# Kernel optimization log

Hardware: AMD Instinct MI355X
Metric: run time of the kernel (lower is better)

The kernel has to match this reference:

```python
import jax, jax.numpy as jnp
import numpy as np

HEADS = 12

def setup_inputs() -> dict:
    key = jax.random.key(0)
    k1, k2, k3 = jax.random.split(key, 3)
    b, n, d = 8, 1024, 768
    x = jax.random.normal(k1, (b, n, d), dtype=jnp.float32)
    # xavier_uniform-like init for linear weights
    lim_qkv = float(np.sqrt(6.0 / (d + 3 * d)))
    W_qkv = jax.random.uniform(k2, (3 * d, d), dtype=jnp.float32, minval=-lim_qkv, maxval=lim_qkv)
    b_qkv = jnp.zeros((3 * d,), dtype=jnp.float32)
    lim_o = float(np.sqrt(6.0 / (d + d)))
    W_out = jax.random.uniform(k3, (d, d), dtype=jnp.float32, minval=-lim_o, maxval=lim_o)
    b_out = jnp.zeros((d,), dtype=jnp.float32)
    return {"x": x, "W_qkv": W_qkv, "b_qkv": b_qkv, "W_out": W_out, "b_out": b_out}

def reference(x, W_qkv, b_qkv, W_out, b_out):
    b, n, d = x.shape
    h = HEADS
    hd = d // h
    scale = d ** (-0.5)  # NOTE: original scales by dim**-0.5, not head_dim**-0.5
    qkv = x @ W_qkv.T + b_qkv                      # [b, n, 3d]
    q, k, v = jnp.split(qkv, 3, axis=-1)           # each [b, n, d]
    def to_heads(t):
        return t.reshape(b, n, h, hd).transpose(0, 2, 1, 3)  # [b, h, n, hd]
    q, k, v = to_heads(q), to_heads(k), to_heads(v)
    dots = jnp.einsum('bhid,bhjd->bhij', q, k) * scale       # [b, h, n, n]
    attn = jax.nn.softmax(dots, axis=-1)
    out = jnp.einsum('bhij,bhjd->bhid', attn, v)             # [b, h, n, hd]
    out = out.transpose(0, 2, 1, 3).reshape(b, n, d)
    return out @ W_out.T + b_out
```

## Files before the change

kernel.cpp:

```cpp
#include <hip/hip_runtime.h>
#include <stdint.h>

typedef __bf16 bf16x8 __attribute__((ext_vector_type(8)));
typedef float  f32x4  __attribute__((ext_vector_type(4)));
typedef unsigned short u16;

#define AS1 __attribute__((address_space(1)))
#define AS3 __attribute__((address_space(3)))
#define G2L(gp, lp) __builtin_amdgcn_global_load_lds( \
    (const AS1 unsigned int*)(uintptr_t)(gp), \
    (AS3 unsigned int*)(uintptr_t)(lp), 16, 0, 0)

static __device__ __forceinline__ u16 f32_to_bf16(float f) {
    unsigned u = __float_as_uint(f);
    u += 0x7fffu + ((u >> 16) & 1u);
    return (u16)(u >> 16);
}

static __device__ __forceinline__ unsigned pack_bf16(float lo, float hi) {
    return (unsigned)f32_to_bf16(lo) | ((unsigned)f32_to_bf16(hi) << 16);
}

static __device__ __forceinline__ float fast_exp2(float x) {
    return __builtin_amdgcn_exp2f(x);
}

static __device__ __forceinline__ f32x4 mfma16(bf16x8 a, bf16x8 b, f32x4 c) {
    return __builtin_amdgcn_mfma_f32_16x16x32_bf16(a, b, c, 0, 0, 0);
}

__global__ void cvt3_k(const float* __restrict__ a, const float* __restrict__ b,
                       const float* __restrict__ c, u16* __restrict__ out) {
    const int i = blockIdx.x * blockDim.x + threadIdx.x;
    const float* src; int off;
    if (i < 1572864)      { src = a; off = 0; }
    else if (i < 2015232) { src = b; off = 1572864; }
    else                  { src = c; off = 2015232; }
    const float4 v = reinterpret_cast<const float4*>(src)[i - off];
    reinterpret_cast<uint2*>(out)[i] = make_uint2(pack_bf16(v.x, v.y), pack_bf16(v.z, v.w));
}

template<int OUTF32>
__global__ __launch_bounds__(256, 2) void gemm_bt_k(const u16* __restrict__ A, const u16* __restrict__ B,
                                                    const float* __restrict__ bias, void* __restrict__ Cp,
                                                    int M, int N, int K, int nbx) {
    __shared__ __align__(16) u16 As[2][128 * 64];
    __shared__ __align__(16) u16 Bs[2][128 * 64];
    const int id = blockIdx.x;
    const int cpx = gridDim.x >> 3;
    const int swz = (id & 7) * cpx + (id >> 3);
    const int bx = swz % nbx, by = swz / nbx;
    const int t = threadIdx.x, w = t >> 6, l = t & 63, lr = l & 15, lg = l >> 4;
    const int wr = w >> 1, wc = w & 1;
    const long rowBase = (long)by * 128;
    const long colBase = (long)bx * 128;

    const f32x4 z = {0.f, 0.f, 0.f, 0.f};
    f32x4 acc[4][4];
    #pragma unroll
    for (int m = 0; m < 4; ++m)
        #pragma unroll
        for (int n = 0; n < 4; ++n) acc[m][n] = z;

    const int kSteps = K >> 6;
    #pragma unroll
    for (int i = 0; i < 4; ++i) {
        const int c = i * 256 + t, row = c >> 3, ch = c & 7;
        const int sch = ch ^ (row & 7);
        G2L(A + (rowBase + row) * K + sch * 8, &As[0][(i * 256 + w * 64) * 8]);
        G2L(B + (colBase + row) * K + sch * 8, &Bs[0][(i * 256 + w * 64) * 8]);
    }
    for (int kt = 0; kt < kSteps; ++kt) {
        const int cur = kt & 1;
        asm volatile("s_waitcnt vmcnt(0)" ::: "memory");
        __builtin_amdgcn_sched_barrier(0);
        __builtin_amdgcn_s_barrier();
        __builtin_amdgcn_sched_barrier(0);
        if (kt + 1 < kSteps) {
            const int k0 = (kt + 1) << 6;
            #pragma unroll
            for (int i = 0; i < 4; ++i) {
                const int c = i * 256 + t, row = c >> 3, ch = c & 7;
                const int sch = ch ^ (row & 7);
                G2L(A + (rowBase + row) * K + k0 + sch * 8, &As[cur ^ 1][(i * 256 + w * 64) * 8]);
                G2L(B + (colBase + row) * K + k0 + sch * 8, &Bs[cur ^ 1][(i * 256 + w * 64) * 8]);
            }
        }
        __builtin_amdgcn_sched_barrier(0);
        #pragma unroll
        for (int kk = 0; kk < 2; ++kk) {
            bf16x8 af[4], bfr[4];
            #pragma unroll
            for (int m = 0; m < 4; ++m) {
                const int row = wr * 64 + m * 16 + lr;
                af[m] = *reinterpret_cast<const bf16x8*>(&As[cur][row * 64 + (((kk * 4 + lg) ^ (lr & 7)) << 3)]);
            }
            #pragma unroll
            for (int n = 0; n < 4; ++n) {
                const int row = wc * 64 + n * 16 + lr;
                bfr[n] = *reinterpret_cast<const bf16x8*>(&Bs[cur][row * 64 + (((kk * 4 + lg) ^ (lr & 7)) << 3)]);
            }
            #pragma unroll
            for (int m = 0; m < 4; ++m)
                #pragma unroll
                for (int n = 0; n < 4; ++n) acc[m][n] = mfma16(af[m], bfr[n], acc[m][n]);
        }
    }
    #pragma unroll
    for (int n = 0; n < 4; ++n) {
        const long gc = colBase + wc * 64 + n * 16 + lr;
        const float bv = bias[gc];
        #pragma unroll
        for (int m = 0; m < 4; ++m) {
            const long gr = rowBase + wr * 64 + m * 16 + lg * 4;
            #pragma unroll
            for (int r = 0; r < 4; ++r) {
                const float v = acc[m][n][r] + bv;
                if (OUTF32) reinterpret_cast<float*>(Cp)[(gr + r) * N + gc] = v;
                else        reinterpret_cast<u16*>(Cp)[(gr + r) * N + gc] = f32_to_bf16(v);
            }
        }
    }
}

__global__ __launch_bounds__(256) void transpose_v_k(const u16* __restrict__ qkv, u16* __restrict__ vt) {
    const int bh = blockIdx.y, b = bh / 12, h = bh % 12;
    const int nt = blockIdx.x;
    __shared__ __align__(16) u16 Ts[64][72];
    const int t = threadIdx.x;
    const int rr = t >> 2;
    #pragma unroll
    for (int i = 0; i < 2; ++i) {
        const int ch = (t & 3) + i * 4;
        const u16* src = qkv + (long)(b * 1024 + nt * 64 + rr) * 2304 + 1536 + h * 64 + ch * 8;
        *reinterpret_cast<uint4*>(&Ts[rr][ch * 8]) = *reinterpret_cast<const uint4*>(src);
    }
    __syncthreads();
    #pragma unroll
    for (int i = 0; i < 2; ++i) {
        const int ch = (t & 3) + i * 4;
        u16 vals[8];
        #pragma unroll
        for (int j = 0; j < 8; ++j)
            vals[j] = Ts[(j & 3) * 16 + ch * 2 + (j >> 2)][rr];
        u16* dst = vt + (long)(bh * 64 + rr) * 1024 + nt * 64 + ch * 8;
        *reinterpret_cast<uint4*>(dst) = *reinterpret_cast<const uint4*>(vals);
    }
}

__global__ __launch_bounds__(256, 3) void attn_k(const u16* __restrict__ qkv, const u16* __restrict__ vt,
                                                 u16* __restrict__ outp) {
    const int id = blockIdx.x;
    const int bh = id % 96, qt = id / 96;
    const int b = bh / 12, h = bh % 12;
    const int t = threadIdx.x, w = t >> 6, l = t & 63, lr = l & 15, lg = l >> 4;
    __shared__ __align__(16) u16 Ks[2][64 * 64];
    __shared__ __align__(16) u16 Vts[2][64 * 64];
    __shared__ __align__(16) u16 Ps[8192];

    const u16* kb = qkv + 768 + h * 64;
    const u16* vb = vt + (long)bh * 64 * 1024;

    #pragma unroll
    for (int i = 0; i < 2; ++i) {
        const int c = (i * 4 + w) * 64 + l;
        const int row = c >> 3, sch = (c & 7) ^ (row & 7);
        G2L(kb + (long)(b * 1024 + row) * 2304 + sch * 8, &Ks[0][(i * 4 + w) * 512]);
        G2L(vb + (long)row * 1024 + sch * 8, &Vts[0][(i * 4 + w) * 512]);
    }
    #pragma unroll
    for (int j = 0; j < 4; ++j) {
        const int c = j * 256 + t, row = c >> 3, ch = c & 7;
        const uint4 q = *reinterpret_cast<const uint4*>(
            qkv + (long)(b * 1024 + qt * 128 + row) * 2304 + h * 64 + ch * 8);
        *reinterpret_cast<uint4*>(&Ps[row * 64 + ((ch ^ (row & 7)) << 3)]) = q;
    }
    __syncthreads();
    bf16x8 aq[2][2];
    #pragma unroll
    for (int qg = 0; qg < 2; ++qg)
        #pragma unroll
        for (int kk = 0; kk < 2; ++kk)
            aq[qg][kk] = *reinterpret_cast<const bf16x8*>(
                &Ps[(qg * 64 + w * 16 + lr) * 64 + (((kk * 4 + lg) ^ (lr & 7)) << 3)]);

    const f32x4 z = {0.f, 0.f, 0.f, 0.f};
    f32x4 o[2][4];
    #pragma unroll
    for (int qg = 0; qg < 2; ++qg)
        #pragma unroll
        for (int n = 0; n < 4; ++n) o[qg][n] = z;
    float lacc[2][4] = {{0.f, 0.f, 0.f, 0.f}, {0.f, 0.f, 0.f, 0.f}};
    const float sc2 = 0.052058773f;

    for (int kt = 0; kt < 16; ++kt) {
        const int cur = kt & 1;
        asm volatile("s_waitcnt vmcnt(0)" ::: "memory");
        __builtin_amdgcn_sched_barrier(0);
        __builtin_amdgcn_s_barrier();
        __builtin_amdgcn_sched_barrier(0);
        if (kt < 15) {
            const int ktn = kt + 1;
            #pragma unroll
            for (int i = 0; i < 2; ++i) {
                const int c = (i * 4 + w) * 64 + l;
                const int row = c >> 3, sch = (c & 7) ^ (row & 7);
                G2L(kb + (long)(b * 1024 + ktn * 64 + row) * 2304 + sch * 8, &Ks[cur ^ 1][(i * 4 + w) * 512]);
                G2L(vb + (long)row * 1024 + ktn * 64 + sch * 8, &Vts[cur ^ 1][(i * 4 + w) * 512]);
            }
        }
        __builtin_amdgcn_sched_barrier(0);
        f32x4 s[2][4];
        #pragma unroll
        for (int qg = 0; qg < 2; ++qg)
            #pragma unroll
            for (int kc = 0; kc < 4; ++kc) s[qg][kc] = z;
        #pragma unroll
        for (int kk = 0; kk < 2; ++kk) {
            #pragma unroll
            for (int kc = 0; kc < 4; ++kc) {
                const int row = kc * 16 + lr;
                bf16x8 bk = *reinterpret_cast<const bf16x8*>(&Ks[cur][row * 64 + (((kk * 4 + lg) ^ (lr & 7)) << 3)]);
                s[0][kc] = mfma16(aq[0][kk], bk, s[0][kc]);
                s[1][kc] = mfma16(aq[1][kk], bk, s[1][kc]);
            }
        }
        #pragma unroll
        for (int qg = 0; qg < 2; ++qg) {
            #pragma unroll
            for (int r = 0; r < 4; ++r) {
                const float p0 = fast_exp2(s[qg][0][r] * sc2);
                const float p1 = fast_exp2(s[qg][1][r] * sc2);
                const float p2 = fast_exp2(s[qg][2][r] * sc2);
                const float p3 = fast_exp2(s[qg][3][r] * sc2);
                lacc[qg][r] += (p0 + p1) + (p2 + p3);
                const unsigned w0 = pack_bf16(p0, p1);
                const unsigned w1 = pack_bf16(p2, p3);
                const int q = lg * 4 + r;
                const int csw = (lr >> 1) ^ (q & 7);
                *reinterpret_cast<uint2*>(&Ps[w * 2048 + qg * 1024 + q * 64 + csw * 8 + (lr & 1) * 4]) =
                    make_uint2(w0, w1);
            }
        }
        #pragma unroll
        for (int kk = 0; kk < 2; ++kk) {
            const int swzk = ((kk * 4 + lg) ^ (lr & 7)) << 3;
            bf16x8 pa0 = *reinterpret_cast<const bf16x8*>(&Ps[w * 2048 + lr * 64 + swzk]);
            bf16x8 pa1 = *reinterpret_cast<const bf16x8*>(&Ps[w * 2048 + 1024 + lr * 64 + swzk]);
            #pragma unroll
            for (int n = 0; n < 4; ++n) {
                const int row = n * 16 + lr;
                bf16x8 vbf = *reinterpret_cast<const bf16x8*>(&Vts[cur][row * 64 + swzk]);
                o[0][n] = mfma16(pa0, vbf, o[0][n]);
                o[1][n] = mfma16(pa1, vbf, o[1][n]);
            }
        }
    }
    #pragma unroll
    for (int qg = 0; qg < 2; ++qg) {
        #pragma unroll
        for (int r = 0; r < 4; ++r) {
            float rs = lacc[qg][r];
            #pragma unroll
            for (int off = 1; off < 16; off <<= 1) rs += __shfl_xor(rs, off, 64);
            lacc[qg][r] = rs;
        }
        const int qrow = qt * 128 + qg * 64 + w * 16 + lg * 4;
        #pragma unroll
        for (int n = 0; n < 4; ++n) {
            #pragma unroll
            for (int r = 0; r < 4; ++r) {
                const float v = o[qg][n][r] / lacc[qg][r];
                outp[(long)(b * 1024 + qrow + r) * 768 + h * 64 + n * 16 + lr] = f32_to_bf16(v);
            }
        }
    }
}

extern "C" void kernel_launch(void* const* d_in, const int* in_sizes, int n_in,
                              void* d_out, int out_size, void* d_ws, size_t ws_size,
                              hipStream_t stream) {
    (void)in_sizes; (void)n_in; (void)out_size; (void)ws_size;
    const float* x    = (const float*)d_in[0];
    const float* Wqkv = (const float*)d_in[1];
    const float* bqkv = (const float*)d_in[2];
    const float* Wout = (const float*)d_in[3];
    const float* bout = (const float*)d_in[4];

    u16* xb   = (u16*)d_ws;
    u16* Wqb  = xb  + 6291456;
    u16* Wob  = Wqb + 1769472;
    u16* qkv  = Wob + 589824;
    u16* vtb  = qkv + 18874368;
    u16* attn = vtb + 6291456;

    cvt3_k<<<8448, 256, 0, stream>>>(x, Wqkv, Wout, xb);

    gemm_bt_k<0><<<1152, 256, 0, stream>>>(xb, Wqb, bqkv, qkv, 8192, 2304, 768, 18);
    transpose_v_k<<<dim3(16, 96), 256, 0, stream>>>(qkv, vtb);
    attn_k<<<768, 256, 0, stream>>>(qkv, vtb, attn);
    gemm_bt_k<1><<<384, 256, 0, stream>>>(attn, Wob, bout, d_out, 8192, 768, 768, 6);
}
```

Measured before the change: 114.4 us.

## Keep softmax probabilities in registers via transposed QK MFMA and fold scale into QKV GEMM

The attention kernel now computes S^T (K as the A operand), so each lane's exp'd scores already form the A-operand layout for the PV MFMA. This removes the per-tile LDS round trip through Ps and the Q staging in LDS. Row sums are computed by an MFMA against a ones vector instead of a shuffle reduction, and V is transposed with a matching key permutation so the register layout lines up. The softmax scale (with log2e) is folded into the Q columns in the QKV GEMM epilogue, which means Q is scaled before being rounded to bf16 and the stored Q precision changes slightly.

```diff
diff --git a/kernel.cpp b/kernel.cpp
--- a/kernel.cpp
+++ b/kernel.cpp
@@ -43,7 +43,7 @@
 template<int OUTF32>
 __global__ __launch_bounds__(256, 2) void gemm_bt_k(const u16* __restrict__ A, const u16* __restrict__ B,
                                                     const float* __restrict__ bias, void* __restrict__ Cp,
-                                                    int M, int N, int K, int nbx) {
+                                                    int M, int N, int K, int nbx, int qcols, float qsc) {
     __shared__ __align__(16) u16 As[2][128 * 64];
     __shared__ __align__(16) u16 Bs[2][128 * 64];
     const int id = blockIdx.x;
@@ -110,12 +110,13 @@
     for (int n = 0; n < 4; ++n) {
         const long gc = colBase + wc * 64 + n * 16 + lr;
         const float bv = bias[gc];
+        const float csc = (gc < qcols) ? qsc : 1.0f;
         #pragma unroll
         for (int m = 0; m < 4; ++m) {
             const long gr = rowBase + wr * 64 + m * 16 + lg * 4;
             #pragma unroll
             for (int r = 0; r < 4; ++r) {
-                const float v = acc[m][n][r] + bv;
+                const float v = (acc[m][n][r] + bv) * csc;
                 if (OUTF32) reinterpret_cast<float*>(Cp)[(gr + r) * N + gc] = v;
                 else        reinterpret_cast<u16*>(Cp)[(gr + r) * N + gc] = f32_to_bf16(v);
             }
@@ -142,7 +143,7 @@
         u16 vals[8];
         #pragma unroll
         for (int j = 0; j < 8; ++j)
-            vals[j] = Ts[(j & 3) * 16 + ch * 2 + (j >> 2)][rr];
+            vals[j] = Ts[(ch >> 2) * 32 + (j >> 2) * 16 + (ch & 3) * 4 + (j & 3)][rr];
         u16* dst = vt + (long)(bh * 64 + rr) * 1024 + nt * 64 + ch * 8;
         *reinterpret_cast<uint4*>(dst) = *reinterpret_cast<const uint4*>(vals);
     }
@@ -156,7 +157,6 @@
     const int t = threadIdx.x, w = t >> 6, l = t & 63, lr = l & 15, lg = l >> 4;
     __shared__ __align__(16) u16 Ks[2][64 * 64];
     __shared__ __align__(16) u16 Vts[2][64 * 64];
-    __shared__ __align__(16) u16 Ps[8192];
 
     const u16* kb = qkv + 768 + h * 64;
     const u16* vb = vt + (long)bh * 64 * 1024;
@@ -168,31 +168,28 @@
         G2L(kb + (long)(b * 1024 + row) * 2304 + sch * 8, &Ks[0][(i * 4 + w) * 512]);
         G2L(vb + (long)row * 1024 + sch * 8, &Vts[0][(i * 4 + w) * 512]);
     }
-    #pragma unroll
-    for (int j = 0; j < 4; ++j) {
-        const int c = j * 256 + t, row = c >> 3, ch = c & 7;
-        const uint4 q = *reinterpret_cast<const uint4*>(
-            qkv + (long)(b * 1024 + qt * 128 + row) * 2304 + h * 64 + ch * 8);
-        *reinterpret_cast<uint4*>(&Ps[row * 64 + ((ch ^ (row & 7)) << 3)]) = q;
-    }
-    __syncthreads();
+    const u16* qb = qkv + (long)(b * 1024 + qt * 128 + w * 32) * 2304 + h * 64;
     bf16x8 aq[2][2];
     #pragma unroll
-    for (int qg = 0; qg < 2; ++qg)
+    for (int qf = 0; qf < 2; ++qf)
         #pragma unroll
         for (int kk = 0; kk < 2; ++kk)
-            aq[qg][kk] = *reinterpret_cast<const bf16x8*>(
-                &Ps[(qg * 64 + w * 16 + lr) * 64 + (((kk * 4 + lg) ^ (lr & 7)) << 3)]);
+            aq[qf][kk] = *reinterpret_cast<const bf16x8*>(qb + (long)(qf * 16 + lr) * 2304 + (kk * 4 + lg) * 8);
 
     const f32x4 z = {0.f, 0.f, 0.f, 0.f};
     f32x4 o[2][4];
-    #pragma unroll
-    for (int qg = 0; qg < 2; ++qg)
-        #pragma unroll
-        for (int n = 0; n < 4; ++n) o[qg][n] = z;
-    float lacc[2][4] = {{0.f, 0.f, 0.f, 0.f}, {0.f, 0.f, 0.f, 0.f}};
-    const float sc2 = 0.052058773f;
-
+    f32x4 dacc[2];
+    #pragma unroll
+    for (int qf = 0; qf < 2; ++qf) {
+        #pragma unroll
+        for (int n = 0; n < 4; ++n) o[qf][n] = z;
+        dacc[qf] = z;
+    }
+    const unsigned one2 = 0x3F803F80u;
+    uint4 onesu = make_uint4(one2, one2, one2, one2);
+    const bf16x8 ones = *reinterpret_cast<const bf16x8*>(&onesu);
+
+    #pragma unroll 2
     for (int kt = 0; kt < 16; ++kt) {
         const int cur = kt & 1;
         asm volatile("s_waitcnt vmcnt(0)" ::: "memory");
@@ -210,68 +207,61 @@
             }
         }
         __builtin_amdgcn_sched_barrier(0);
-        f32x4 s[2][4];
-        #pragma unroll
-        for (int qg = 0; qg < 2; ++qg)
-            #pragma unroll
-            for (int kc = 0; kc < 4; ++kc) s[qg][kc] = z;
+        f32x4 s[4][2];
+        #pragma unroll
+        for (int kc = 0; kc < 4; ++kc)
+            #pragma unroll
+            for (int qf = 0; qf < 2; ++qf) s[kc][qf] = z;
         #pragma unroll
         for (int kk = 0; kk < 2; ++kk) {
             #pragma unroll
             for (int kc = 0; kc < 4; ++kc) {
                 const int row = kc * 16 + lr;
                 bf16x8 bk = *reinterpret_cast<const bf16x8*>(&Ks[cur][row * 64 + (((kk * 4 + lg) ^ (lr & 7)) << 3)]);
-                s[0][kc] = mfma16(aq[0][kk], bk, s[0][kc]);
-                s[1][kc] = mfma16(aq[1][kk], bk, s[1][kc]);
-            }
-        }
-        #pragma unroll
-        for (int qg = 0; qg < 2; ++qg) {
-            #pragma unroll
-            for (int r = 0; r < 4; ++r) {
-                const float p0 = fast_exp2(s[qg][0][r] * sc2);
-                const float p1 = fast_exp2(s[qg][1][r] * sc2);
-                const float p2 = fast_exp2(s[qg][2][r] * sc2);
-                const float p3 = fast_exp2(s[qg][3][r] * sc2);
-                lacc[qg][r] += (p0 + p1) + (p2 + p3);
-                const unsigned w0 = pack_bf16(p0, p1);
-                const unsigned w1 = pack_bf16(p2, p3);
-                const int q = lg * 4 + r;
-                const int csw = (lr >> 1) ^ (q & 7);
-                *reinterpret_cast<uint2*>(&Ps[w * 2048 + qg * 1024 + q * 64 + csw * 8 + (lr & 1) * 4]) =
-                    make_uint2(w0, w1);
-            }
-        }
-        #pragma unroll
-        for (int kk = 0; kk < 2; ++kk) {
-            const int swzk = ((kk * 4 + lg) ^ (lr & 7)) << 3;
-            bf16x8 pa0 = *reinterpret_cast<const bf16x8*>(&Ps[w * 2048 + lr * 64 + swzk]);
-            bf16x8 pa1 = *reinterpret_cast<const bf16x8*>(&Ps[w * 2048 + 1024 + lr * 64 + swzk]);
+                s[kc][0] = mfma16(bk, aq[0][kk], s[kc][0]);
+                s[kc][1] = mfma16(bk, aq[1][kk], s[kc][1]);
+            }
+        }
+        #pragma unroll
+        for (int qf = 0; qf < 2; ++qf) {
+            float pv[4][4];
+            #pragma unroll
+            for (int kc = 0; kc < 4; ++kc)
+                #pragma unroll
+                for (int r = 0; r < 4; ++r)
+                    pv[kc][r] = fast_exp2(s[kc][qf][r]);
+            uint4 u0, u1;
+            u0.x = pack_bf16(pv[0][0], pv[0][1]); u0.y = pack_bf16(pv[0][2], pv[0][3]);
+            u0.z = pack_bf16(pv[1][0], pv[1][1]); u0.w = pack_bf16(pv[1][2], pv[1][3]);
+            u1.x = pack_bf16(pv[2][0], pv[2][1]); u1.y = pack_bf16(pv[2][2], pv[2][3]);
+            u1.z = pack_bf16(pv[3][0], pv[3][1]); u1.w = pack_bf16(pv[3][2], pv[3][3]);
+            bf16x8 pa0 = *reinterpret_cast<bf16x8*>(&u0);
+            bf16x8 pa1 = *reinterpret_cast<bf16x8*>(&u1);
+            dacc[qf] = mfma16(pa0, ones, dacc[qf]);
+            dacc[qf] = mfma16(pa1, ones, dacc[qf]);
+            #pragma unroll
+            for (int kk = 0; kk < 2; ++kk) {
+                const bf16x8 pa = kk ? pa1 : pa0;
+                const int swzk = ((kk * 4 + lg) ^ (lr & 7)) << 3;
+                #pragma unroll
+                for (int n = 0; n < 4; ++n) {
+                    const int row = n * 16 + lr;
+                    bf16x8 vbf = *reinterpret_cast<const bf16x8*>(&Vts[cur][row * 64 + swzk]);
+                    o[qf][n] = mfma16(pa, vbf, o[qf][n]);
+                }
+            }
+        }
+    }
+    #pragma unroll
+    for (int qf = 0; qf < 2; ++qf) {
+        const int qrow = qt * 128 + w * 32 + qf * 16 + lg * 4;
+        #pragma unroll
+        for (int r = 0; r < 4; ++r) {
+            const float inv = 1.0f / dacc[qf][r];
             #pragma unroll
             for (int n = 0; n < 4; ++n) {
-                const int row = n * 16 + lr;
-                bf16x8 vbf = *reinterpret_cast<const bf16x8*>(&Vts[cur][row * 64 + swzk]);
-                o[0][n] = mfma16(pa0, vbf, o[0][n]);
-                o[1][n] = mfma16(pa1, vbf, o[1][n]);
-            }
-        }
-    }
-    #pragma unroll
-    for (int qg = 0; qg < 2; ++qg) {
-        #pragma unroll
-        for (int r = 0; r < 4; ++r) {
-            float rs = lacc[qg][r];
-            #pragma unroll
-            for (int off = 1; off < 16; off <<= 1) rs += __shfl_xor(rs, off, 64);
-            lacc[qg][r] = rs;
-        }
-        const int qrow = qt * 128 + qg * 64 + w * 16 + lg * 4;
-        #pragma unroll
-        for (int n = 0; n < 4; ++n) {
-            #pragma unroll
-            for (int r = 0; r < 4; ++r) {
-                const float v = o[qg][n][r] / lacc[qg][r];
-                outp[(long)(b * 1024 + qrow + r) * 768 + h * 64 + n * 16 + lr] = f32_to_bf16(v);
+                outp[(long)(b * 1024 + qrow + r) * 768 + h * 64 + n * 16 + lr] =
+                    f32_to_bf16(o[qf][n][r] * inv);
             }
         }
     }
@@ -294,10 +284,12 @@
     u16* vtb  = qkv + 18874368;
     u16* attn = vtb + 6291456;
 
+    const float sc2 = 0.052058773f;
+
     cvt3_k<<<8448, 256, 0, stream>>>(x, Wqkv, Wout, xb);
 
-    gemm_bt_k<0><<<1152, 256, 0, stream>>>(xb, Wqb, bqkv, qkv, 8192, 2304, 768, 18);
+    gemm_bt_k<0><<<1152, 256, 0, stream>>>(xb, Wqb, bqkv, qkv, 8192, 2304, 768, 18, 768, sc2);
     transpose_v_k<<<dim3(16, 96), 256, 0, stream>>>(qkv, vtb);
     attn_k<<<768, 256, 0, stream>>>(qkv, vtb, attn);
-    gemm_bt_k<1><<<384, 256, 0, stream>>>(attn, Wob, bout, d_out, 8192, 768, 768, 6);
-}
+    gemm_bt_k<1><<<384, 256, 0, stream>>>(attn, Wob, bout, d_out, 8192, 768, 768, 6, 0, 1.0f);
+}
```

New measurement: 102.8 us, median of 2. -10.2%, faster.
